# Kernel optimization log

Measured on AMD Instinct MI355X. Metric: run time of the kernel, lower is better.

Reference implementation:

```python
import jax, jax.numpy as jnp
import numpy as np

N = 6144
IN_F = 256
OUT_F = 64
ALPHA = 0.2  # leaky relu slope
NEG_INF = -9e15
ADJ_DENSITY = 0.01


def setup_inputs() -> dict:
    key = jax.random.key(0)
    kx, ka, kw, kat, ks, ke = jax.random.split(key, 6)
    x = jax.random.normal(kx, (N, IN_F), dtype=jnp.float32)
    adj = (jax.random.uniform(ka, (N, N)) < ADJ_DENSITY).astype(jnp.float32)
    adj = adj.at[jnp.arange(N), jnp.arange(N)].set(0.0)
    # xavier-uniform-ish init scale (gain 1.414)
    def xavier(k, shape):
        fan_in, fan_out = shape[0], shape[1]
        lim = 1.414 * np.sqrt(6.0 / (fan_in + fan_out))
        return jax.random.uniform(k, shape, minval=-lim, maxval=lim, dtype=jnp.float32)
    W = xavier(kw, (IN_F, OUT_F))
    a = xavier(kat, (2 * OUT_F, 1))
    W_si = xavier(ks, (1, 1))
    W_ei = xavier(ke, (1, 1))
    return {"x": x, "adj": adj, "W": W, "a": a, "W_si": W_si, "W_ei": W_ei}


def reference(x, adj, W, a, W_si, W_ei):
    # h: [N, F_out]
    h = x @ W
    # additive GAT score: e[i,j] = leakyrelu(Wh1[i] + Wh2[j])
    Wh1 = h @ a[:OUT_F, :]           # [N, 1]
    Wh2 = h @ a[OUT_F:, :]           # [N, 1]
    e = jax.nn.leaky_relu(Wh1 + Wh2.T, negative_slope=ALPHA)  # [N, N]
    # adjacency-power topology bias
    adj2 = adj @ adj
    adj3 = adj2 @ adj
    adj_w = adj + adj2 + adj3
    adj_w = adj_w.at[jnp.arange(N), jnp.arange(N)].set(0.0)
    e = jnp.abs(W_ei) * e + jnp.abs(W_si) * adj_w
    # masked softmax over neighbors (row-wise)
    scores = jnp.where(adj > 0, e, NEG_INF)
    attention = jax.nn.softmax(scores, axis=1)
    # dropout omitted (eval mode / training=False)
    h_prime = attention @ h
    return jax.nn.elu(h_prime)
```

## Files before the change

### kernel.cpp

```cpp
#include <hip/hip_runtime.h>
#include <math.h>

#define N 6144
#define MAXD 128
#define NWORDS 96
#define NW32 192

typedef unsigned long long u64;
typedef unsigned int u32;
typedef unsigned short u16;

#define BADD7(c, in) do { \
    u32 _cy = (in), _x;                         \
    _x = c[0] & _cy; c[0] ^= _cy; _cy = _x;     \
    _x = c[1] & _cy; c[1] ^= _cy; _cy = _x;     \
    _x = c[2] & _cy; c[2] ^= _cy; _cy = _x;     \
    _x = c[3] & _cy; c[3] ^= _cy; _cy = _x;     \
    _x = c[4] & _cy; c[4] ^= _cy; _cy = _x;     \
    _x = c[5] & _cy; c[5] ^= _cy; _cy = _x;     \
    c[6] ^= _cy;                                \
} while (0)

#define BMERGE(a, b) do { \
    u32 _cin = 0, _tp, _co;                                         \
    _Pragma("unroll")                                               \
    for (int _p = 0; _p < 7; ++_p) {                                \
        _tp = a[_p] ^ b[_p];                                        \
        _co = (a[_p] & b[_p]) | (_cin & _tp);                       \
        a[_p] = _tp ^ _cin; _cin = _co;                             \
    }                                                               \
} while (0)

__global__ __launch_bounds__(256) void k_gemm_h(
    const float* __restrict__ x, const float* __restrict__ W,
    const float* __restrict__ a,
    float* __restrict__ h, float* __restrict__ Wh1, float* __restrict__ Wh2,
    int* __restrict__ col_cnt)
{
    int gid = blockIdx.x * 256 + threadIdx.x;
    if (gid < N) col_cnt[gid] = 0;

    __shared__ float Wl[256 * 64];
    int t = threadIdx.x;
    #pragma unroll
    for (int c = 0; c < 64; ++c) Wl[c * 256 + t] = W[c * 256 + t];
    __syncthreads();

    int w = t >> 6, lane = t & 63;
    int i0 = blockIdx.x * 32 + w * 8;
    const float* xr = x + (long)i0 * 256;

    float acc[8] = {0.f, 0.f, 0.f, 0.f, 0.f, 0.f, 0.f, 0.f};
    for (int k0 = 0; k0 < 256; k0 += 4) {
        float4 xv[8];
        #pragma unroll
        for (int r = 0; r < 8; ++r)
            xv[r] = *(const float4*)(xr + (long)r * 256 + k0);
        #pragma unroll
        for (int kk = 0; kk < 4; ++kk) {
            float wv = Wl[(k0 + kk) * 64 + lane];
            #pragma unroll
            for (int r = 0; r < 8; ++r) {
                float xs = (kk == 0) ? xv[r].x : (kk == 1) ? xv[r].y
                         : (kk == 2) ? xv[r].z : xv[r].w;
                acc[r] = fmaf(xs, wv, acc[r]);
            }
        }
    }

    #pragma unroll
    for (int r = 0; r < 8; ++r) {
        int i = i0 + r;
        h[(long)i * 64 + lane] = acc[r];
        float s1 = acc[r] * a[lane];
        float s2 = acc[r] * a[64 + lane];
        #pragma unroll
        for (int off = 32; off; off >>= 1) {
            s1 += __shfl_xor(s1, off, 64);
            s2 += __shfl_xor(s2, off, 64);
        }
        if (lane == 0) { Wh1[i] = s1; Wh2[i] = s2; }
    }
}

__global__ __launch_bounds__(256) void k_build(
    const float* __restrict__ adj,
    u64* __restrict__ rowbits, int* __restrict__ row_cnt, int* __restrict__ row_list,
    int* __restrict__ col_cnt, int* __restrict__ col_list)
{
    int i = blockIdx.x;
    int t = threadIdx.x, w = t >> 6, lane = t & 63;
    __shared__ int cnt;
    if (t == 0) cnt = 0;
    __syncthreads();

    const float* ar = adj + (long)i * N;

    float v[24];
    #pragma unroll
    for (int c = 0; c < 24; ++c)
        v[c] = __builtin_nontemporal_load(ar + c * 256 + t);

    u64 mask[24];
    #pragma unroll
    for (int c = 0; c < 24; ++c) mask[c] = __ballot(v[c] != 0.0f);

    #pragma unroll
    for (int c = 0; c < 24; ++c) {
        if (lane == 0) rowbits[(long)i * NWORDS + c * 4 + w] = mask[c];
        int base = 0;
        if (lane == 0 && mask[c]) base = atomicAdd(&cnt, __popcll(mask[c]));
        base = __shfl(base, 0, 64);
        if ((mask[c] >> lane) & 1ull) {
            int rank = __popcll(mask[c] & ((1ull << lane) - 1ull));
            int s = base + rank;
            int j = c * 256 + t;
            if (s < MAXD) row_list[(long)i * MAXD + s] = j;
            int sc = atomicAdd(&col_cnt[j], 1);
            if (sc < MAXD) col_list[(long)j * MAXD + sc] = i;
        }
    }
    __syncthreads();
    if (t == 0) row_cnt[i] = cnt < 127 ? cnt : 127;
}

__global__ __launch_bounds__(192) void k_attn(
    const float* __restrict__ h, const float* __restrict__ Wh1, const float* __restrict__ Wh2,
    const u64* __restrict__ rowbits,
    const int* __restrict__ row_cnt, const int* __restrict__ row_list,
    const int* __restrict__ col_cnt, const int* __restrict__ col_list,
    const float* __restrict__ W_si, const float* __restrict__ W_ei,
    float* __restrict__ out)
{
    __shared__ u16 adj2t[32 * 193];
    __shared__ int nbr[MAXD];
    __shared__ int ccbuf[MAXD];
    __shared__ float lrbuf[MAXD];
    __shared__ float ebuf[MAXD];
    __shared__ float part[192];
    __shared__ float sh_max, sh_sum;

    int i = blockIdx.x;
    int t = threadIdx.x, w = t >> 6, lane = t & 63;
    int deg = row_cnt[i];

    if (deg == 0) {
        float acc = 0.f;
        for (int r = w; r < N; r += 3) acc += h[(long)r * 64 + lane];
        part[t] = acc;
        __syncthreads();
        if (w == 0) {
            float s = part[lane] + part[64 + lane] + part[128 + lane];
            s *= (1.0f / N);
            out[(long)i * 64 + lane] = s > 0.f ? s : expm1f(s);
        }
        return;
    }

    float aWei = fabsf(W_ei[0]);
    float aWsi = fabsf(W_si[0]);

    if (t < deg) {
        int j = row_list[(long)i * MAXD + t];
        nbr[t] = j;
        int cc = col_cnt[j];
        ccbuf[t] = cc < MAXD ? cc : MAXD;
        float z = Wh1[i] + Wh2[j];
        lrbuf[t] = aWei * (z > 0.f ? z : 0.2f * z);
    }
    __syncthreads();

    {
        const u32* rb32 = (const u32*)rowbits;
        u32 p0[7] = {0,0,0,0,0,0,0};
        u32 p1[7] = {0,0,0,0,0,0,0};
        u32 p2[7] = {0,0,0,0,0,0,0};
        u32 p3[7] = {0,0,0,0,0,0,0};
        int m = 0;
        for (; m + 4 <= deg; m += 4) {
            int b0 = __builtin_amdgcn_readfirstlane(nbr[m])     * NW32;
            int b1 = __builtin_amdgcn_readfirstlane(nbr[m + 1]) * NW32;
            int b2 = __builtin_amdgcn_readfirstlane(nbr[m + 2]) * NW32;
            int b3 = __builtin_amdgcn_readfirstlane(nbr[m + 3]) * NW32;
            u32 w0 = rb32[b0 + t];
            u32 w1 = rb32[b1 + t];
            u32 w2 = rb32[b2 + t];
            u32 w3 = rb32[b3 + t];
            BADD7(p0, w0); BADD7(p1, w1); BADD7(p2, w2); BADD7(p3, w3);
        }
        for (; m < deg; ++m) {
            int b0 = __builtin_amdgcn_readfirstlane(nbr[m]) * NW32;
            u32 w0 = rb32[b0 + t];
            BADD7(p0, w0);
        }
        BMERGE(p0, p1);
        BMERGE(p2, p3);
        BMERGE(p0, p2);
        #pragma unroll
        for (int j2 = 0; j2 < 32; ++j2) {
            u32 cnt = ((p0[0]>>j2)&1u) | (((p0[1]>>j2)&1u)<<1) | (((p0[2]>>j2)&1u)<<2)
                    | (((p0[3]>>j2)&1u)<<3) | (((p0[4]>>j2)&1u)<<4) | (((p0[5]>>j2)&1u)<<5)
                    | (((p0[6]>>j2)&1u)<<6);
            adj2t[j2 * 193 + t] = (u16)cnt;
        }
    }
    __syncthreads();

    {
        int g = t >> 3, sub = t & 7;
        for (int e = g; e < deg; e += 24) {
            int j = nbr[e];
            int cc = ccbuf[e];
            const int* cl = col_list + (long)j * MAXD;
            u32 a3 = 0;
            for (int q = sub; q < cc; q += 8) {
                int k = cl[q];
                a3 += (u32)adj2t[(k & 31) * 193 + (k >> 5)];
            }
            a3 += __shfl_xor(a3, 1, 64);
            a3 += __shfl_xor(a3, 2, 64);
            a3 += __shfl_xor(a3, 4, 64);
            if (sub == 0) {
                u32 a2 = (u32)adj2t[(j & 31) * 193 + (j >> 5)];
                ebuf[e] = lrbuf[e] + aWsi * (float)(1u + a2 + a3);
            }
        }
    }
    __syncthreads();

    if (w == 0) {
        float v = -3.4e38f;
        for (int idx = lane; idx < deg; idx += 64) v = fmaxf(v, ebuf[idx]);
        #pragma unroll
        for (int off = 32; off; off >>= 1) v = fmaxf(v, __shfl_xor(v, off, 64));
        if (lane == 0) sh_max = v;
    }
    __syncthreads();
    if (t < deg) ebuf[t] = expf(ebuf[t] - sh_max);
    __syncthreads();
    if (w == 0) {
        float s = 0.f;
        for (int idx = lane; idx < deg; idx += 64) s += ebuf[idx];
        #pragma unroll
        for (int off = 32; off; off >>= 1) s += __shfl_xor(s, off, 64);
        if (lane == 0) sh_sum = s;
    }
    __syncthreads();

    float accf = 0.f;
    for (int e = w; e < deg; e += 3)
        accf = fmaf(ebuf[e], h[(long)nbr[e] * 64 + lane], accf);
    part[t] = accf;
    __syncthreads();
    if (w == 0) {
        float s = part[lane] + part[64 + lane] + part[128 + lane];
        s /= sh_sum;
        out[(long)i * 64 + lane] = s > 0.f ? s : expm1f(s);
    }
}

extern "C" void kernel_launch(void* const* d_in, const int* in_sizes, int n_in,
                              void* d_out, int out_size, void* d_ws, size_t ws_size,
                              hipStream_t stream) {
    const float* x    = (const float*)d_in[0];
    const float* adj  = (const float*)d_in[1];
    const float* W    = (const float*)d_in[2];
    const float* a    = (const float*)d_in[3];
    const float* W_si = (const float*)d_in[4];
    const float* W_ei = (const float*)d_in[5];
    float* out = (float*)d_out;

    char* ws = (char*)d_ws;
    size_t off = 0;
    auto alloc = [&](size_t bytes) -> void* {
        void* p = ws + off;
        off += (bytes + 255) & ~(size_t)255;
        return p;
    };
    u64*   rowbits  = (u64*)  alloc((size_t)N * NWORDS * sizeof(u64));
    float* h        = (float*)alloc((size_t)N * 64 * sizeof(float));
    float* Wh1      = (float*)alloc((size_t)N * sizeof(float));
    float* Wh2      = (float*)alloc((size_t)N * sizeof(float));
    int*   row_cnt  = (int*)  alloc((size_t)N * sizeof(int));
    int*   row_list = (int*)  alloc((size_t)N * MAXD * sizeof(int));
    int*   col_cnt  = (int*)  alloc((size_t)N * sizeof(int));
    int*   col_list = (int*)  alloc((size_t)N * MAXD * sizeof(int));

    k_gemm_h<<<N / 32, 256, 0, stream>>>(x, W, a, h, Wh1, Wh2, col_cnt);
    k_build <<<N, 256, 0, stream>>>(adj, rowbits, row_cnt, row_list, col_cnt, col_list);
    k_attn  <<<N, 192, 0, stream>>>(h, Wh1, Wh2, rowbits, row_cnt, row_list,
                                    col_cnt, col_list, W_si, W_ei, out);
}
```

Before: 343.4 us.

## Use 15-input carry-save compressor for bit-sliced adj² counts and byte-packed LDS

Replaces the four ripple-carry bit-sliced accumulators with one 15-to-4 carry-save compressor tree per group of 15 neighbor rows. This cuts the bitwise ops per added row and issues 15 independent global loads per iteration. Neighbor indices are read straight from row_list, which removes a barrier. The per-thread counts are transposed into a byte-packed LDS table with a multiply-mask trick instead of 32 shift/or sequences into u16 storage, and the adj³ lookups index that table by byte. The cost is more registers for the 15 loaded words and a padded tail iteration with masked loads.

```diff
diff --git a/kernel.cpp b/kernel.cpp
--- a/kernel.cpp
+++ b/kernel.cpp
@@ -8,28 +8,38 @@
 
 typedef unsigned long long u64;
 typedef unsigned int u32;
-typedef unsigned short u16;
-
-#define BADD7(c, in) do { \
-    u32 _cy = (in), _x;                         \
-    _x = c[0] & _cy; c[0] ^= _cy; _cy = _x;     \
-    _x = c[1] & _cy; c[1] ^= _cy; _cy = _x;     \
-    _x = c[2] & _cy; c[2] ^= _cy; _cy = _x;     \
-    _x = c[3] & _cy; c[3] ^= _cy; _cy = _x;     \
-    _x = c[4] & _cy; c[4] ^= _cy; _cy = _x;     \
-    _x = c[5] & _cy; c[5] ^= _cy; _cy = _x;     \
-    c[6] ^= _cy;                                \
-} while (0)
-
-#define BMERGE(a, b) do { \
-    u32 _cin = 0, _tp, _co;                                         \
-    _Pragma("unroll")                                               \
-    for (int _p = 0; _p < 7; ++_p) {                                \
-        _tp = a[_p] ^ b[_p];                                        \
-        _co = (a[_p] & b[_p]) | (_cin & _tp);                       \
-        a[_p] = _tp ^ _cin; _cin = _co;                             \
-    }                                                               \
-} while (0)
+typedef unsigned char u8;
+
+#define FA(s, c, a, b, ci) { u32 _t = (a) ^ (b); (s) = _t ^ (ci); (c) = ((a) & (b)) | ((ci) & _t); }
+
+template <int START>
+__device__ __forceinline__ void badd_from(u32* p, u32 cy) {
+    #pragma unroll
+    for (int q = START; q < 6; ++q) { u32 x = p[q] & cy; p[q] ^= cy; cy = x; }
+    p[6] ^= cy;
+}
+
+__device__ __forceinline__ void csa15(u32* p, const u32* x) {
+    u32 s0,c0,s1,c1,s2,c2,s3,c3,s4,c4;
+    FA(s0,c0, x[0], x[1], x[2]);
+    FA(s1,c1, x[3], x[4], x[5]);
+    FA(s2,c2, x[6], x[7], x[8]);
+    FA(s3,c3, x[9], x[10], x[11]);
+    FA(s4,c4, x[12], x[13], x[14]);
+    u32 t0,d0,u0,d1;
+    FA(t0,d0, s0, s1, s2);
+    FA(u0,d1, s3, s4, t0);
+    u32 e0,f0,e1,f1,e2,f2;
+    FA(e0,f0, c0, c1, c2);
+    FA(e1,f1, c3, c4, d0);
+    FA(e2,f2, e0, e1, d1);
+    u32 g0,h0;
+    FA(g0,h0, f0, f1, f2);
+    badd_from<0>(p, u0);
+    badd_from<1>(p, e2);
+    badd_from<2>(p, g0);
+    badd_from<3>(p, h0);
+}
 
 __global__ __launch_bounds__(256) void k_gemm_h(
     const float* __restrict__ x, const float* __restrict__ W,
@@ -132,7 +142,7 @@
     const float* __restrict__ W_si, const float* __restrict__ W_ei,
     float* __restrict__ out)
 {
-    __shared__ u16 adj2t[32 * 193];
+    __shared__ u32 adj2p[8 * 256];
     __shared__ int nbr[MAXD];
     __shared__ int ccbuf[MAXD];
     __shared__ float lrbuf[MAXD];
@@ -168,43 +178,48 @@
         float z = Wh1[i] + Wh2[j];
         lrbuf[t] = aWei * (z > 0.f ? z : 0.2f * z);
     }
-    __syncthreads();
 
     {
         const u32* rb32 = (const u32*)rowbits;
-        u32 p0[7] = {0,0,0,0,0,0,0};
-        u32 p1[7] = {0,0,0,0,0,0,0};
-        u32 p2[7] = {0,0,0,0,0,0,0};
-        u32 p3[7] = {0,0,0,0,0,0,0};
+        const int* rl = row_list + (long)i * MAXD;
+        u32 p[7] = {0,0,0,0,0,0,0};
+
         int m = 0;
-        for (; m + 4 <= deg; m += 4) {
-            int b0 = __builtin_amdgcn_readfirstlane(nbr[m])     * NW32;
-            int b1 = __builtin_amdgcn_readfirstlane(nbr[m + 1]) * NW32;
-            int b2 = __builtin_amdgcn_readfirstlane(nbr[m + 2]) * NW32;
-            int b3 = __builtin_amdgcn_readfirstlane(nbr[m + 3]) * NW32;
-            u32 w0 = rb32[b0 + t];
-            u32 w1 = rb32[b1 + t];
-            u32 w2 = rb32[b2 + t];
-            u32 w3 = rb32[b3 + t];
-            BADD7(p0, w0); BADD7(p1, w1); BADD7(p2, w2); BADD7(p3, w3);
-        }
-        for (; m < deg; ++m) {
-            int b0 = __builtin_amdgcn_readfirstlane(nbr[m]) * NW32;
-            u32 w0 = rb32[b0 + t];
-            BADD7(p0, w0);
-        }
-        BMERGE(p0, p1);
-        BMERGE(p2, p3);
-        BMERGE(p0, p2);
-        #pragma unroll
-        for (int j2 = 0; j2 < 32; ++j2) {
-            u32 cnt = ((p0[0]>>j2)&1u) | (((p0[1]>>j2)&1u)<<1) | (((p0[2]>>j2)&1u)<<2)
-                    | (((p0[3]>>j2)&1u)<<3) | (((p0[4]>>j2)&1u)<<4) | (((p0[5]>>j2)&1u)<<5)
-                    | (((p0[6]>>j2)&1u)<<6);
-            adj2t[j2 * 193 + t] = (u16)cnt;
-        }
-    }
-    __syncthreads();
+        for (; m + 15 <= deg; m += 15) {
+            u32 x[15];
+            #pragma unroll
+            for (int q = 0; q < 15; ++q) {
+                int j = rl[m + q];
+                x[q] = rb32[(long)j * NW32 + t];
+            }
+            csa15(p, x);
+        }
+        if (m < deg) {
+            u32 x[15];
+            #pragma unroll
+            for (int q = 0; q < 15; ++q) {
+                int mq = m + q;
+                int j = rl[mq < deg ? mq : 0];
+                u32 vv = rb32[(long)j * NW32 + t];
+                x[q] = (mq < deg) ? vv : 0u;
+            }
+            csa15(p, x);
+        }
+
+        #pragma unroll
+        for (int g = 0; g < 8; ++g) {
+            u32 acc = 0;
+            #pragma unroll
+            for (int pl = 0; pl < 7; ++pl) {
+                u32 nib = (p[pl] >> (4 * g)) & 0xFu;
+                acc += ((nib * 0x00204081u) & 0x01010101u) << pl;
+            }
+            adj2p[g * 256 + t] = acc;
+        }
+    }
+    __syncthreads();
+
+    const u8* adj2b = (const u8*)adj2p;
 
     {
         int g = t >> 3, sub = t & 7;
@@ -215,13 +230,13 @@
             u32 a3 = 0;
             for (int q = sub; q < cc; q += 8) {
                 int k = cl[q];
-                a3 += (u32)adj2t[(k & 31) * 193 + (k >> 5)];
+                a3 += (u32)adj2b[(((k >> 2) & 7) << 10) | (((k >> 5) << 2) | (k & 3))];
             }
             a3 += __shfl_xor(a3, 1, 64);
             a3 += __shfl_xor(a3, 2, 64);
             a3 += __shfl_xor(a3, 4, 64);
             if (sub == 0) {
-                u32 a2 = (u32)adj2t[(j & 31) * 193 + (j >> 5)];
+                u32 a2 = (u32)adj2b[(((j >> 2) & 7) << 10) | (((j >> 5) << 2) | (j & 3))];
                 ebuf[e] = lrbuf[e] + aWsi * (float)(1u + a2 + a3);
             }
         }
```

After: 328.5 us. 4.3% less time.
